# Kernel tuning notes

Measured on AMD Instinct MI355X. Metric: run time of the kernel, lower is better.

## Reference

```python
import jax, jax.numpy as jnp
import numpy as np

N_NODES = 100000
N_EDGES = 1600000
N_GRAPHS = 256
IN_DIM, HID = 30, 40

def setup_inputs() -> dict:
    key = jax.random.key(0)
    ks = jax.random.split(key, 12)
    x = jax.random.normal(ks[0], (N_NODES, IN_DIM), dtype=jnp.float32)
    edge_index = jax.random.randint(ks[1], (2, N_EDGES), 0, N_NODES, dtype=jnp.int64)
    batch = jnp.sort(jax.random.randint(ks[2], (N_NODES,), 0, N_GRAPHS, dtype=jnp.int64))
    def glorot(k, shape):
        lim = float(np.sqrt(6.0 / (shape[0] + shape[1])))
        return jax.random.uniform(k, shape, dtype=jnp.float32, minval=-lim, maxval=lim)
    return {
        'x': x, 'edge_index': edge_index, 'batch': batch,
        'W1': glorot(ks[3], (IN_DIM, HID)), 'b1': jnp.zeros((HID,), jnp.float32),
        'W2': glorot(ks[4], (HID, HID)),    'b2': jnp.zeros((HID,), jnp.float32),
        'W3': glorot(ks[5], (HID, HID)),    'b3': jnp.zeros((HID,), jnp.float32),
        'lin_w': glorot(ks[6], (HID, 1)),   'lin_b': jnp.zeros((1,), jnp.float32),
    }

def _gcn_layer(x, src, dst, norm, W, b, n_nodes):
    # x: [N, Fin] -> [N, Fout]; fused gather-matmul-scatter form of GCNConv
    h = x @ W                                   # dense transform first (Fout small)
    msg = h[src] * norm[:, None]                # [E+N, Fout] gather + edge scale
    out = jax.ops.segment_sum(msg, dst, num_segments=n_nodes)
    return out + b

def reference(x, edge_index, batch, W1, b1, W2, b2, W3, b3, lin_w, lin_b):
    n = x.shape[0]
    loops = jnp.arange(n, dtype=edge_index.dtype)
    src = jnp.concatenate([edge_index[0], loops])  # add self loops (GCNConv default)
    dst = jnp.concatenate([edge_index[1], loops])
    deg = jax.ops.segment_sum(jnp.ones_like(dst, dtype=x.dtype), dst, num_segments=n)
    dinv = jax.lax.rsqrt(jnp.maximum(deg, 1.0))    # deg >= 1 thanks to self loops
    norm = dinv[src] * dinv[dst]

    h = jax.nn.relu(_gcn_layer(x, src, dst, norm, W1, b1, n))  # dropout inactive (eval)
    h = jax.nn.relu(_gcn_layer(h, src, dst, norm, W2, b2, n))
    h = jax.nn.relu(_gcn_layer(h, src, dst, norm, W3, b3, n))

    # global_mean_pool over graphs
    g_sum = jax.ops.segment_sum(h, batch, num_segments=N_GRAPHS)
    cnt = jax.ops.segment_sum(jnp.ones((n,), h.dtype), batch, num_segments=N_GRAPHS)
    g = g_sum / jnp.maximum(cnt, 1.0)[:, None]
    return g @ lin_w + lin_b                      # [N_GRAPHS, 1]
```

## Files before the change

kernel.cpp:

```cpp
#include <hip/hip_runtime.h>

#define HID 40
#define RBKT 196
#define BSH 9
#define CAP 12288
#define EPB 4096


typedef __attribute__((ext_vector_type(4))) unsigned uv4;
typedef __attribute__((ext_vector_type(8))) __bf16 bf16x8;
typedef __attribute__((ext_vector_type(8))) unsigned short usv8;
typedef __attribute__((ext_vector_type(4))) float f32x4;

__device__ inline unsigned pack2_bf16(float a, float b) {
    unsigned ua = __float_as_uint(a);
    unsigned ub = __float_as_uint(b);
    ua = (ua + 0x7fffu + ((ua >> 16) & 1u)) >> 16;
    ub = (ub + 0x7fffu + ((ub >> 16) & 1u)) & 0xffff0000u;
    return ua | ub;
}

__device__ inline void acc8_bf16(float* acc, uint4 v) {
    acc[0] += __uint_as_float(v.x << 16);
    acc[1] += __uint_as_float(v.x & 0xffff0000u);
    acc[2] += __uint_as_float(v.y << 16);
    acc[3] += __uint_as_float(v.y & 0xffff0000u);
    acc[4] += __uint_as_float(v.z << 16);
    acc[5] += __uint_as_float(v.z & 0xffff0000u);
    acc[6] += __uint_as_float(v.w << 16);
    acc[7] += __uint_as_float(v.w & 0xffff0000u);
}

__device__ inline void wprep_dev(const float* __restrict__ W,
                                 unsigned* __restrict__ wtab, int INF, int l) {
    int lr = l & 15, lg = l >> 4;
    int kstn = (INF > 32) ? 2 : 1;
    for (int kst = 0; kst < kstn; kst++) {
        for (int ct = 0; ct < 3; ct++) {
            unsigned short v[8];
            #pragma unroll
            for (int i = 0; i < 8; i++) {
                int kb = kst * 32 + lg * 8 + i;
                int col = ct * 16 + lr;
                float f = (kb < INF && col < 40) ? W[kb * 40 + col] : 0.f;
                v[i] = (unsigned short)(pack2_bf16(f, 0.f) & 0xffffu);
            }
            uint4 u;
            u.x = (unsigned)v[0] | ((unsigned)v[1] << 16);
            u.y = (unsigned)v[2] | ((unsigned)v[3] << 16);
            u.z = (unsigned)v[4] | ((unsigned)v[5] << 16);
            u.w = (unsigned)v[6] | ((unsigned)v[7] << 16);
            reinterpret_cast<uint4*>(wtab)[(kst * 3 + ct) * 64 + l] = u;
        }
    }
}

__global__ void prep_kernel(int* __restrict__ bucket_cnt, float* __restrict__ g_sum, int G,
                            const float* __restrict__ W1, const float* __restrict__ W2,
                            const float* __restrict__ W3,
                            unsigned* __restrict__ wtab1, unsigned* __restrict__ wtab2,
                            unsigned* __restrict__ wtab3) {
    int t = threadIdx.x;
    if (t < RBKT) bucket_cnt[t] = 0;
    if (t < G) g_sum[t] = 0.f;
    int w = t >> 6, l = t & 63;
    if (w == 1) wprep_dev(W1, wtab1, 30, l);
    else if (w == 2) wprep_dev(W2, wtab2, 40, l);
    else if (w == 3) wprep_dev(W3, wtab3, 40, l);
}


__global__ __launch_bounds__(256) void binA_kernel(
        const int* __restrict__ esrc, const int* __restrict__ edst, int E,
        int* __restrict__ bucket_cnt, int* __restrict__ bucket_data) {
    __shared__ int cnt_l[RBKT];
    __shared__ int base_l[RBKT];
    int t = threadIdx.x;
    for (int b = t; b < RBKT; b += 256) cnt_l[b] = 0;
    __syncthreads();
    int e0 = blockIdx.x * EPB;
    int e1 = min(e0 + EPB, E);
    for (int e = e0 + t; e < e1; e += 256) {
        atomicAdd(&cnt_l[edst[e] >> BSH], 1);
    }
    __syncthreads();
    for (int b = t; b < RBKT; b += 256) {
        int c = cnt_l[b];
        base_l[b] = (c > 0) ? atomicAdd(&bucket_cnt[b], c) : 0;
        cnt_l[b] = 0;
    }
    __syncthreads();
    for (int e = e0 + t; e < e1; e += 256) {
        int d = edst[e];
        int s = esrc[e];
        int b = d >> BSH;
        int off = base_l[b] + atomicAdd(&cnt_l[b], 1);
        if (off < CAP) bucket_data[(size_t)b * CAP + off] = (s << BSH) | (d & 511);
    }
}

__global__ void scan_buckets_kernel(const int* __restrict__ cnt, int* __restrict__ base) {
    __shared__ int s[256];
    int t = threadIdx.x;
    int c = (t < RBKT) ? min(cnt[t], CAP) : 0;
    s[t] = c;
    __syncthreads();
    for (int off = 1; off < 256; off <<= 1) {
        int y = (t >= off) ? s[t - off] : 0;
        __syncthreads();
        s[t] += y;
        __syncthreads();
    }
    if (t < RBKT) base[t] = s[t] - c;
    if (t == RBKT - 1) base[RBKT] = s[t];
}

__global__ __launch_bounds__(256) void buildB_kernel(
        const int* __restrict__ bucket_cnt, const int* __restrict__ bucket_base,
        const int* __restrict__ bucket_data,
        int* __restrict__ rowptr, int* __restrict__ mid, int* __restrict__ csr,
        float* __restrict__ dinv, int n, int half) {
    __shared__ int deg_l[512];
    __shared__ int deg_lo[512];
    __shared__ int off_lo[512];
    __shared__ int off_hi[512];
    __shared__ int ps[256];
    int r = blockIdx.x;
    int t = threadIdx.x;
    int cnt = min(bucket_cnt[r], CAP);
    int base = bucket_base[r];
    int node0 = r << BSH;
    int nr = min(512, n - node0);
    for (int i = t; i < 512; i += 256) { deg_l[i] = 0; deg_lo[i] = 0; }
    __syncthreads();
    const int* data = bucket_data + (size_t)r * CAP;
    for (int e = t; e < cnt; e += 256) {
        int v = data[e];
        atomicAdd(&deg_l[v & 511], 1);
        if ((v >> BSH) < half) atomicAdd(&deg_lo[v & 511], 1);
    }
    __syncthreads();
    int a0 = deg_l[2 * t], a1 = deg_l[2 * t + 1];
    ps[t] = a0 + a1;
    __syncthreads();
    for (int off = 1; off < 256; off <<= 1) {
        int y = (t >= off) ? ps[t - off] : 0;
        __syncthreads();
        ps[t] += y;
        __syncthreads();
    }
    int excl = ps[t] - (a0 + a1);
    off_lo[2 * t] = excl;
    off_lo[2 * t + 1] = excl + a0;
    off_hi[2 * t] = excl + deg_lo[2 * t];
    off_hi[2 * t + 1] = excl + a0 + deg_lo[2 * t + 1];
    __syncthreads();
    for (int i = t; i < nr; i += 256) {
        int rp = base + off_lo[i];
        rowptr[node0 + i] = rp;
        mid[node0 + i] = rp + deg_lo[i];
        dinv[node0 + i] = rsqrtf((float)(deg_l[i] + 1));
    }
    if (r == RBKT - 1 && t == 0) rowptr[n] = base + cnt;
    __syncthreads();
    for (int e = t; e < cnt; e += 256) {
        int v = data[e];
        int s = v >> BSH;
        int d = v & 511;
        int p = (s < half) ? atomicAdd(&off_lo[d], 1) : atomicAdd(&off_hi[d], 1);
        csr[base + p] = s;
    }
}


__global__ __launch_bounds__(256) void scale_bf16_kernel(
        const float* __restrict__ x, const float* __restrict__ dinv,
        unsigned* __restrict__ xs, int n) {
    int t = blockIdx.x * blockDim.x + threadIdx.x;
    int i = t >> 4, p = t & 15;
    if (i >= n) return;
    float a = 0.f, b = 0.f;
    if (p < 15) {
        float d = dinv[i];
        a = x[i * 30 + 2 * p] * d;
        b = x[i * 30 + 2 * p + 1] * d;
    }
    xs[(size_t)i * 16 + p] = pack2_bf16(a, b);
}

template <int INF, int RQ, bool POOL>
__global__ __launch_bounds__(64 * RQ) void fused_layer_kernel(
        const unsigned* __restrict__ xs, const unsigned* __restrict__ wtab,
        const int* __restrict__ rowptr, const int* __restrict__ mid,
        const int* __restrict__ csr, const float* __restrict__ dinv,
        const float* __restrict__ bias, const float* __restrict__ lin_w,
        const int* __restrict__ batch,
        unsigned* __restrict__ out, float* __restrict__ g_sum, int n) {
    constexpr int KST = (INF > 32) ? 2 : 1;
    constexpr int NT  = 64 * RQ;
    constexpr int TS  = (RQ == 4) ? 5 : 7;
    __shared__ uint4 tile[64 * TS];
    __shared__ float sarr[POOL ? 64 : 1];
    __shared__ unsigned ost[POOL ? 1 : 64 * 21];
    const int tid = threadIdx.x;

    {
        const int node_l = tid / RQ, q = tid - node_l * RQ;
        const int gi = blockIdx.x * 64 + node_l;
        if (gi < n) {
            const uint4* tab = reinterpret_cast<const uint4*>(xs);
            float acc[8];
            {
                uint4 v = tab[(size_t)gi * RQ + q];
                acc[0] = __uint_as_float(v.x << 16);
                acc[1] = __uint_as_float(v.x & 0xffff0000u);
                acc[2] = __uint_as_float(v.y << 16);
                acc[3] = __uint_as_float(v.y & 0xffff0000u);
                acc[4] = __uint_as_float(v.z << 16);
                acc[5] = __uint_as_float(v.z & 0xffff0000u);
                acc[6] = __uint_as_float(v.w << 16);
                acc[7] = __uint_as_float(v.w & 0xffff0000u);
            }
            int e0 = rowptr[gi], m = mid[gi], e1 = rowptr[gi + 1];
            int e = e0;
            for (; e + 4 <= m; e += 4) {
                int s0 = csr[e], s1 = csr[e + 1], s2 = csr[e + 2], s3 = csr[e + 3];
                uint4 v0 = tab[(size_t)s0 * RQ + q];
                uint4 v1 = tab[(size_t)s1 * RQ + q];
                uint4 v2 = tab[(size_t)s2 * RQ + q];
                uint4 v3 = tab[(size_t)s3 * RQ + q];
                acc8_bf16(acc, v0);
                acc8_bf16(acc, v1);
                acc8_bf16(acc, v2);
                acc8_bf16(acc, v3);
            }
            for (; e < m; e++) acc8_bf16(acc, tab[(size_t)csr[e] * RQ + q]);
            for (; e + 4 <= e1; e += 4) {
                int s0 = csr[e], s1 = csr[e + 1], s2 = csr[e + 2], s3 = csr[e + 3];
                uint4 v0 = tab[(size_t)s0 * RQ + q];
                uint4 v1 = tab[(size_t)s1 * RQ + q];
                uint4 v2 = tab[(size_t)s2 * RQ + q];
                uint4 v3 = tab[(size_t)s3 * RQ + q];
                acc8_bf16(acc, v0);
                acc8_bf16(acc, v1);
                acc8_bf16(acc, v2);
                acc8_bf16(acc, v3);
            }
            for (; e < e1; e++) acc8_bf16(acc, tab[(size_t)csr[e] * RQ + q]);
            float d = dinv[gi];
            uint4 o;
            o.x = pack2_bf16(acc[0] * d, acc[1] * d);
            o.y = pack2_bf16(acc[2] * d, acc[3] * d);
            o.z = pack2_bf16(acc[4] * d, acc[5] * d);
            o.w = pack2_bf16(acc[6] * d, acc[7] * d);
            tile[node_l * TS + q] = o;
        }
    }
    __syncthreads();

    const int wv = tid >> 6, l = tid & 63, lr = l & 15, lg = l >> 4;
    if (wv < 4) {
        const uv4* wt = reinterpret_cast<const uv4*>(wtab);
        usv8 wf[KST][3];
        #pragma unroll
        for (int kst = 0; kst < KST; kst++) {
            #pragma unroll
            for (int ct = 0; ct < 3; ct++) {
                wf[kst][ct] = __builtin_bit_cast(usv8, wt[(kst * 3 + ct) * 64 + l]);
            }
        }
        const int node0 = blockIdx.x * 64 + wv * 16;
        const int arow_l = wv * 16 + lr;
        bf16x8 a0 = __builtin_bit_cast(bf16x8, tile[arow_l * TS + lg]);
        bf16x8 a1;
        if constexpr (KST == 2) {
            uint4 z4 = {0u, 0u, 0u, 0u};
            uint4 a1q = (lg == 0) ? tile[arow_l * TS + 4] : z4;
            a1 = __builtin_bit_cast(bf16x8, a1q);
        }
        f32x4 acc[3];
        #pragma unroll
        for (int ct = 0; ct < 3; ct++) {
            f32x4 z = {0.f, 0.f, 0.f, 0.f};
            acc[ct] = __builtin_amdgcn_mfma_f32_16x16x32_bf16(
                a0, __builtin_bit_cast(bf16x8, wf[0][ct]), z, 0, 0, 0);
            if constexpr (KST == 2) {
                acc[ct] = __builtin_amdgcn_mfma_f32_16x16x32_bf16(
                    a1, __builtin_bit_cast(bf16x8, wf[1][ct]), acc[ct], 0, 0, 0);
            }
        }
        int noder[4]; float dr[4]; bool vr[4];
        #pragma unroll
        for (int r = 0; r < 4; r++) {
            noder[r] = node0 + lg * 4 + r;
            vr[r] = (noder[r] < n);
            dr[r] = vr[r] ? dinv[noder[r]] : 0.f;
        }
        if (!POOL) {
            #pragma unroll
            for (int ct = 0; ct < 3; ct++) {
                int col = ct * 16 + lr;
                float bc = (col < 40) ? bias[col] : 0.f;
                #pragma unroll
                for (int r = 0; r < 4; r++) {
                    float v = fmaxf(acc[ct][r] + bc, 0.f) * dr[r];
                    float pv = __shfl_xor(v, 1, 64);
                    if (((lr & 1) == 0) && col < 40) {
                        int nl = wv * 16 + lg * 4 + r;
                        ost[nl * 21 + ct * 8 + (lr >> 1)] = pack2_bf16(v, pv);
                    }
                }
            }
        } else {
            float s[4] = {0.f, 0.f, 0.f, 0.f};
            #pragma unroll
            for (int ct = 0; ct < 3; ct++) {
                int col = ct * 16 + lr;
                float bc = (col < 40) ? bias[col] : 0.f;
                float lwv = (col < 40) ? lin_w[col] : 0.f;
                #pragma unroll
                for (int r = 0; r < 4; r++)
                    s[r] += fmaxf(acc[ct][r] + bc, 0.f) * lwv;
            }
            #pragma unroll
            for (int r = 0; r < 4; r++) if (!vr[r]) s[r] = 0.f;
            #pragma unroll
            for (int mask = 1; mask <= 8; mask <<= 1) {
                #pragma unroll
                for (int r = 0; r < 4; r++) s[r] += __shfl_xor(s[r], mask, 64);
            }
            if (lr == 0) {
                #pragma unroll
                for (int r = 0; r < 4; r++) sarr[wv * 16 + lg * 4 + r] = s[r];
            }
        }
    }
    __syncthreads();

    if (!POOL) {
        int blk0 = blockIdx.x * 64;
        int nr = min(64, n - blk0);
        int tot = nr * 5;
        uint4* outq = reinterpret_cast<uint4*>(out) + (size_t)blk0 * 5;
        for (int idx = tid; idx < tot; idx += NT) {
            int nl = idx / 5, c4 = idx - nl * 5;
            uint4 v;
            v.x = ost[nl * 21 + c4 * 4 + 0];
            v.y = ost[nl * 21 + c4 * 4 + 1];
            v.z = ost[nl * 21 + c4 * 4 + 2];
            v.w = ost[nl * 21 + c4 * 4 + 3];
            outq[idx] = v;
        }
    } else {
        if (tid < 64) {
            float ss = sarr[tid];
            int node2 = blockIdx.x * 64 + tid;
            bool v2 = (node2 < n);
            int gg = batch[v2 ? node2 : (n - 1)];
            if (!v2) ss = 0.f;
            int g0 = __shfl(gg, 0, 64);
            if (__all(gg == g0)) {
                #pragma unroll
                for (int off2 = 32; off2 > 0; off2 >>= 1) ss += __shfl_xor(ss, off2, 64);
                if (tid == 0) atomicAdd(&g_sum[g0], ss);
            } else {
                if (v2) atomicAdd(&g_sum[gg], ss);
            }
        }
    }
}

__global__ void finalize_kernel(const float* __restrict__ g_sum,
                                const int* __restrict__ batch,
                                const float* __restrict__ lin_b,
                                float* __restrict__ out, int n, int G) {
    int b = blockIdx.x * blockDim.x + threadIdx.x;
    if (b >= G) return;
    int lo = 0, hi = n;
    while (lo < hi) { int m = (lo + hi) >> 1; if (batch[m] < b) lo = m + 1; else hi = m; }
    int lo2 = lo, hi2 = n;
    while (lo2 < hi2) { int m = (lo2 + hi2) >> 1; if (batch[m] < b + 1) lo2 = m + 1; else hi2 = m; }
    int cnt = lo2 - lo;
    out[b] = g_sum[b] / (float)(cnt > 0 ? cnt : 1) + lin_b[0];
}


static inline size_t align_up(size_t v, size_t a) { return (v + a - 1) / a * a; }

extern "C" void kernel_launch(void* const* d_in, const int* in_sizes, int n_in,
                              void* d_out, int out_size, void* d_ws, size_t ws_size,
                              hipStream_t stream) {
    const float* x      = (const float*)d_in[0];
    const int*   esrc   = (const int*)d_in[1];
    const int*   batch  = (const int*)d_in[2];
    const float* W1     = (const float*)d_in[3];
    const float* b1     = (const float*)d_in[4];
    const float* W2     = (const float*)d_in[5];
    const float* b2     = (const float*)d_in[6];
    const float* W3     = (const float*)d_in[7];
    const float* b3     = (const float*)d_in[8];
    const float* lin_w  = (const float*)d_in[9];
    const float* lin_b  = (const float*)d_in[10];
    float* out = (float*)d_out;

    const int n = in_sizes[0] / 30;
    const int E = in_sizes[1] / 2;
    const int G = out_size;
    const int* edst = esrc + E;

    char* w = (char*)d_ws;
    size_t off = 0;
    auto take = [&](size_t bytes) { size_t o = off; off = align_up(off + bytes, 256); return (void*)(w + o); };
    int*      bucket_cnt  = (int*)take((size_t)RBKT * 4);
    int*      bucket_base = (int*)take((size_t)(RBKT + 1) * 4);
    int*      rowptr      = (int*)take((size_t)(n + 1) * 4);
    int*      mid         = (int*)take((size_t)n * 4);
    float*    dinv        = (float*)take((size_t)n * 4);
    int*      csr         = (int*)take((size_t)E * 4);
    float*    g_sum       = (float*)take((size_t)G * 4);
    unsigned* wtab1       = (unsigned*)take((size_t)3 * 64 * 16);
    unsigned* wtab2       = (unsigned*)take((size_t)6 * 64 * 16);
    unsigned* wtab3       = (unsigned*)take((size_t)6 * 64 * 16);
    size_t bd = (size_t)RBKT * CAP * 4;
    size_t x1 = (size_t)n * 16 * 4;
    void* shared_region = take(bd > x1 ? bd : x1);
    int*      bucket_data = (int*)shared_region;
    unsigned* xs1         = (unsigned*)shared_region;
    unsigned* tbA         = (unsigned*)take((size_t)n * 20 * 4);
    unsigned* tbB         = (unsigned*)take((size_t)n * 20 * 4);
    (void)ws_size;

    prep_kernel<<<1, 256, 0, stream>>>(bucket_cnt, g_sum, G, W1, W2, W3,
                                       wtab1, wtab2, wtab3);

    binA_kernel<<<(E + EPB - 1) / EPB, 256, 0, stream>>>(esrc, edst, E, bucket_cnt, bucket_data);
    scan_buckets_kernel<<<1, 256, 0, stream>>>(bucket_cnt, bucket_base);
    buildB_kernel<<<RBKT, 256, 0, stream>>>(bucket_cnt, bucket_base, bucket_data,
                                            rowptr, mid, csr, dinv, n, n / 2);

    int nblk = (n + 63) / 64;

    scale_bf16_kernel<<<((size_t)n * 16 + 255) / 256, 256, 0, stream>>>(x, dinv, xs1, n);
    fused_layer_kernel<30, 4, false><<<nblk, 256, 0, stream>>>(
        xs1, wtab1, rowptr, mid, csr, dinv, b1, nullptr, nullptr, tbA, nullptr, n);
    fused_layer_kernel<40, 5, false><<<nblk, 320, 0, stream>>>(
        tbA, wtab2, rowptr, mid, csr, dinv, b2, nullptr, nullptr, tbB, nullptr, n);
    fused_layer_kernel<40, 5, true><<<nblk, 320, 0, stream>>>(
        tbB, wtab3, rowptr, mid, csr, dinv, b3, lin_w, batch, nullptr, g_sum, n);

    finalize_kernel<<<1, 256, 0, stream>>>(g_sum, batch, lin_b, out, n, G);
}
```

Measured before the change: 196.3 us.

## Process two nodes per thread group to interleave gathers in fused GCN layers

Each block now handles 128 nodes instead of 64. Every thread group aggregates two nodes (A and B) at once, interleaving their neighbor gathers in lockstep batches of four so more independent loads are in flight. The MFMA stage runs two passes per wave, and the pooling stage uses two wavefronts. Doubling per-thread accumulators raises register pressure and halves the grid size, which may reduce occupancy. Imbalanced degrees between A and B fall back to the serial drain loops.

```diff
diff --git a/kernel.cpp b/kernel.cpp
--- a/kernel.cpp
+++ b/kernel.cpp
@@ -199,31 +199,32 @@
     constexpr int KST = (INF > 32) ? 2 : 1;
     constexpr int NT  = 64 * RQ;
     constexpr int TS  = (RQ == 4) ? 5 : 7;
-    __shared__ uint4 tile[64 * TS];
-    __shared__ float sarr[POOL ? 64 : 1];
-    __shared__ unsigned ost[POOL ? 1 : 64 * 21];
+    __shared__ uint4 tile[128 * TS];
+    __shared__ float sarr[POOL ? 128 : 1];
+    __shared__ unsigned ost[POOL ? 1 : 128 * 21];
     const int tid = threadIdx.x;
+    const uint4* tab = reinterpret_cast<const uint4*>(xs);
 
     {
-        const int node_l = tid / RQ, q = tid - node_l * RQ;
-        const int gi = blockIdx.x * 64 + node_l;
-        if (gi < n) {
-            const uint4* tab = reinterpret_cast<const uint4*>(xs);
-            float acc[8];
-            {
-                uint4 v = tab[(size_t)gi * RQ + q];
-                acc[0] = __uint_as_float(v.x << 16);
-                acc[1] = __uint_as_float(v.x & 0xffff0000u);
-                acc[2] = __uint_as_float(v.y << 16);
-                acc[3] = __uint_as_float(v.y & 0xffff0000u);
-                acc[4] = __uint_as_float(v.z << 16);
-                acc[5] = __uint_as_float(v.z & 0xffff0000u);
-                acc[6] = __uint_as_float(v.w << 16);
-                acc[7] = __uint_as_float(v.w & 0xffff0000u);
-            }
-            int e0 = rowptr[gi], m = mid[gi], e1 = rowptr[gi + 1];
-            int e = e0;
-            for (; e + 4 <= m; e += 4) {
+        const int nl = tid / RQ, q = tid - nl * RQ;
+        const int gA = blockIdx.x * 128 + nl;
+        const int gB = gA + 64;
+        const bool vA = (gA < n), vB = (gB < n);
+        float accA[8] = {0,0,0,0,0,0,0,0};
+        float accB[8] = {0,0,0,0,0,0,0,0};
+        int eA = 0, mA = 0, eA1 = 0, eB = 0, mB = 0, eB1 = 0;
+        if (vA) {
+            uint4 v = tab[(size_t)gA * RQ + q];
+            acc8_bf16(accA, v);
+            eA = rowptr[gA]; mA = mid[gA]; eA1 = rowptr[gA + 1];
+        }
+        if (vB) {
+            uint4 v = tab[(size_t)gB * RQ + q];
+            acc8_bf16(accB, v);
+            eB = rowptr[gB]; mB = mid[gB]; eB1 = rowptr[gB + 1];
+        }
+        auto drain = [&](int e, int end, float* acc) {
+            for (; e + 4 <= end; e += 4) {
                 int s0 = csr[e], s1 = csr[e + 1], s2 = csr[e + 2], s3 = csr[e + 3];
                 uint4 v0 = tab[(size_t)s0 * RQ + q];
                 uint4 v1 = tab[(size_t)s1 * RQ + q];
@@ -234,26 +235,64 @@
                 acc8_bf16(acc, v2);
                 acc8_bf16(acc, v3);
             }
-            for (; e < m; e++) acc8_bf16(acc, tab[(size_t)csr[e] * RQ + q]);
-            for (; e + 4 <= e1; e += 4) {
-                int s0 = csr[e], s1 = csr[e + 1], s2 = csr[e + 2], s3 = csr[e + 3];
-                uint4 v0 = tab[(size_t)s0 * RQ + q];
-                uint4 v1 = tab[(size_t)s1 * RQ + q];
-                uint4 v2 = tab[(size_t)s2 * RQ + q];
-                uint4 v3 = tab[(size_t)s3 * RQ + q];
-                acc8_bf16(acc, v0);
-                acc8_bf16(acc, v1);
-                acc8_bf16(acc, v2);
-                acc8_bf16(acc, v3);
-            }
-            for (; e < e1; e++) acc8_bf16(acc, tab[(size_t)csr[e] * RQ + q]);
-            float d = dinv[gi];
+            for (; e < end; e++) acc8_bf16(acc, tab[(size_t)csr[e] * RQ + q]);
+        };
+        while (eA + 4 <= mA && eB + 4 <= mB) {
+            int a0 = csr[eA], a1 = csr[eA + 1], a2 = csr[eA + 2], a3 = csr[eA + 3];
+            int b0 = csr[eB], b1 = csr[eB + 1], b2 = csr[eB + 2], b3 = csr[eB + 3];
+            uint4 va0 = tab[(size_t)a0 * RQ + q];
+            uint4 vb0 = tab[(size_t)b0 * RQ + q];
+            uint4 va1 = tab[(size_t)a1 * RQ + q];
+            uint4 vb1 = tab[(size_t)b1 * RQ + q];
+            uint4 va2 = tab[(size_t)a2 * RQ + q];
+            uint4 vb2 = tab[(size_t)b2 * RQ + q];
+            uint4 va3 = tab[(size_t)a3 * RQ + q];
+            uint4 vb3 = tab[(size_t)b3 * RQ + q];
+            acc8_bf16(accA, va0); acc8_bf16(accB, vb0);
+            acc8_bf16(accA, va1); acc8_bf16(accB, vb1);
+            acc8_bf16(accA, va2); acc8_bf16(accB, vb2);
+            acc8_bf16(accA, va3); acc8_bf16(accB, vb3);
+            eA += 4; eB += 4;
+        }
+        drain(eA, mA, accA);
+        drain(eB, mB, accB);
+        eA = mA; eB = mB;
+        while (eA + 4 <= eA1 && eB + 4 <= eB1) {
+            int a0 = csr[eA], a1 = csr[eA + 1], a2 = csr[eA + 2], a3 = csr[eA + 3];
+            int b0 = csr[eB], b1 = csr[eB + 1], b2 = csr[eB + 2], b3 = csr[eB + 3];
+            uint4 va0 = tab[(size_t)a0 * RQ + q];
+            uint4 vb0 = tab[(size_t)b0 * RQ + q];
+            uint4 va1 = tab[(size_t)a1 * RQ + q];
+            uint4 vb1 = tab[(size_t)b1 * RQ + q];
+            uint4 va2 = tab[(size_t)a2 * RQ + q];
+            uint4 vb2 = tab[(size_t)b2 * RQ + q];
+            uint4 va3 = tab[(size_t)a3 * RQ + q];
+            uint4 vb3 = tab[(size_t)b3 * RQ + q];
+            acc8_bf16(accA, va0); acc8_bf16(accB, vb0);
+            acc8_bf16(accA, va1); acc8_bf16(accB, vb1);
+            acc8_bf16(accA, va2); acc8_bf16(accB, vb2);
+            acc8_bf16(accA, va3); acc8_bf16(accB, vb3);
+            eA += 4; eB += 4;
+        }
+        drain(eA, eA1, accA);
+        drain(eB, eB1, accB);
+        if (vA) {
+            float d = dinv[gA];
             uint4 o;
-            o.x = pack2_bf16(acc[0] * d, acc[1] * d);
-            o.y = pack2_bf16(acc[2] * d, acc[3] * d);
-            o.z = pack2_bf16(acc[4] * d, acc[5] * d);
-            o.w = pack2_bf16(acc[6] * d, acc[7] * d);
-            tile[node_l * TS + q] = o;
+            o.x = pack2_bf16(accA[0] * d, accA[1] * d);
+            o.y = pack2_bf16(accA[2] * d, accA[3] * d);
+            o.z = pack2_bf16(accA[4] * d, accA[5] * d);
+            o.w = pack2_bf16(accA[6] * d, accA[7] * d);
+            tile[nl * TS + q] = o;
+        }
+        if (vB) {
+            float d = dinv[gB];
+            uint4 o;
+            o.x = pack2_bf16(accB[0] * d, accB[1] * d);
+            o.y = pack2_bf16(accB[2] * d, accB[3] * d);
+            o.z = pack2_bf16(accB[4] * d, accB[5] * d);
+            o.w = pack2_bf16(accB[6] * d, accB[7] * d);
+            tile[(nl + 64) * TS + q] = o;
         }
     }
     __syncthreads();
@@ -269,92 +308,96 @@
                 wf[kst][ct] = __builtin_bit_cast(usv8, wt[(kst * 3 + ct) * 64 + l]);
             }
         }
-        const int node0 = blockIdx.x * 64 + wv * 16;
-        const int arow_l = wv * 16 + lr;
-        bf16x8 a0 = __builtin_bit_cast(bf16x8, tile[arow_l * TS + lg]);
-        bf16x8 a1;
-        if constexpr (KST == 2) {
-            uint4 z4 = {0u, 0u, 0u, 0u};
-            uint4 a1q = (lg == 0) ? tile[arow_l * TS + 4] : z4;
-            a1 = __builtin_bit_cast(bf16x8, a1q);
-        }
-        f32x4 acc[3];
         #pragma unroll
-        for (int ct = 0; ct < 3; ct++) {
-            f32x4 z = {0.f, 0.f, 0.f, 0.f};
-            acc[ct] = __builtin_amdgcn_mfma_f32_16x16x32_bf16(
-                a0, __builtin_bit_cast(bf16x8, wf[0][ct]), z, 0, 0, 0);
+        for (int pass = 0; pass < 2; pass++) {
+            const int tt = wv + pass * 4;
+            const int node0 = blockIdx.x * 128 + tt * 16;
+            const int arow_l = tt * 16 + lr;
+            bf16x8 a0 = __builtin_bit_cast(bf16x8, tile[arow_l * TS + lg]);
+            bf16x8 a1;
             if constexpr (KST == 2) {
-                acc[ct] = __builtin_amdgcn_mfma_f32_16x16x32_bf16(
-                    a1, __builtin_bit_cast(bf16x8, wf[1][ct]), acc[ct], 0, 0, 0);
-            }
-        }
-        int noder[4]; float dr[4]; bool vr[4];
-        #pragma unroll
-        for (int r = 0; r < 4; r++) {
-            noder[r] = node0 + lg * 4 + r;
-            vr[r] = (noder[r] < n);
-            dr[r] = vr[r] ? dinv[noder[r]] : 0.f;
-        }
-        if (!POOL) {
+                uint4 z4 = {0u, 0u, 0u, 0u};
+                uint4 a1q = (lg == 0) ? tile[arow_l * TS + 4] : z4;
+                a1 = __builtin_bit_cast(bf16x8, a1q);
+            }
+            f32x4 acc[3];
             #pragma unroll
             for (int ct = 0; ct < 3; ct++) {
-                int col = ct * 16 + lr;
-                float bc = (col < 40) ? bias[col] : 0.f;
+                f32x4 z = {0.f, 0.f, 0.f, 0.f};
+                acc[ct] = __builtin_amdgcn_mfma_f32_16x16x32_bf16(
+                    a0, __builtin_bit_cast(bf16x8, wf[0][ct]), z, 0, 0, 0);
+                if constexpr (KST == 2) {
+                    acc[ct] = __builtin_amdgcn_mfma_f32_16x16x32_bf16(
+                        a1, __builtin_bit_cast(bf16x8, wf[1][ct]), acc[ct], 0, 0, 0);
+                }
+            }
+            int noder[4]; float dr[4]; bool vr[4];
+            #pragma unroll
+            for (int r = 0; r < 4; r++) {
+                noder[r] = node0 + lg * 4 + r;
+                vr[r] = (noder[r] < n);
+                dr[r] = vr[r] ? dinv[noder[r]] : 0.f;
+            }
+            if (!POOL) {
                 #pragma unroll
-                for (int r = 0; r < 4; r++) {
-                    float v = fmaxf(acc[ct][r] + bc, 0.f) * dr[r];
-                    float pv = __shfl_xor(v, 1, 64);
-                    if (((lr & 1) == 0) && col < 40) {
-                        int nl = wv * 16 + lg * 4 + r;
-                        ost[nl * 21 + ct * 8 + (lr >> 1)] = pack2_bf16(v, pv);
+                for (int ct = 0; ct < 3; ct++) {
+                    int col = ct * 16 + lr;
+                    float bc = (col < 40) ? bias[col] : 0.f;
+                    #pragma unroll
+                    for (int r = 0; r < 4; r++) {
+                        float v = fmaxf(acc[ct][r] + bc, 0.f) * dr[r];
+                        float pv = __shfl_xor(v, 1, 64);
+                        if (((lr & 1) == 0) && col < 40) {
+                            int nl2 = tt * 16 + lg * 4 + r;
+                            ost[nl2 * 21 + ct * 8 + (lr >> 1)] = pack2_bf16(v, pv);
+                        }
                     }
                 }
-            }
-        } else {
-            float s[4] = {0.f, 0.f, 0.f, 0.f};
-            #pragma unroll
-            for (int ct = 0; ct < 3; ct++) {
-                int col = ct * 16 + lr;
-                float bc = (col < 40) ? bias[col] : 0.f;
-                float lwv = (col < 40) ? lin_w[col] : 0.f;
+            } else {
+                float s[4] = {0.f, 0.f, 0.f, 0.f};
                 #pragma unroll
-                for (int r = 0; r < 4; r++)
-                    s[r] += fmaxf(acc[ct][r] + bc, 0.f) * lwv;
-            }
-            #pragma unroll
-            for (int r = 0; r < 4; r++) if (!vr[r]) s[r] = 0.f;
-            #pragma unroll
-            for (int mask = 1; mask <= 8; mask <<= 1) {
+                for (int ct = 0; ct < 3; ct++) {
+                    int col = ct * 16 + lr;
+                    float bc = (col < 40) ? bias[col] : 0.f;
+                    float lwv = (col < 40) ? lin_w[col] : 0.f;
+                    #pragma unroll
+                    for (int r = 0; r < 4; r++)
+                        s[r] += fmaxf(acc[ct][r] + bc, 0.f) * lwv;
+                }
                 #pragma unroll
-                for (int r = 0; r < 4; r++) s[r] += __shfl_xor(s[r], mask, 64);
-            }
-            if (lr == 0) {
+                for (int r = 0; r < 4; r++) if (!vr[r]) s[r] = 0.f;
                 #pragma unroll
-                for (int r = 0; r < 4; r++) sarr[wv * 16 + lg * 4 + r] = s[r];
+                for (int mask = 1; mask <= 8; mask <<= 1) {
+                    #pragma unroll
+                    for (int r = 0; r < 4; r++) s[r] += __shfl_xor(s[r], mask, 64);
+                }
+                if (lr == 0) {
+                    #pragma unroll
+                    for (int r = 0; r < 4; r++) sarr[tt * 16 + lg * 4 + r] = s[r];
+                }
             }
         }
     }
     __syncthreads();
 
     if (!POOL) {
-        int blk0 = blockIdx.x * 64;
-        int nr = min(64, n - blk0);
+        int blk0 = blockIdx.x * 128;
+        int nr = min(128, n - blk0);
         int tot = nr * 5;
         uint4* outq = reinterpret_cast<uint4*>(out) + (size_t)blk0 * 5;
         for (int idx = tid; idx < tot; idx += NT) {
-            int nl = idx / 5, c4 = idx - nl * 5;
+            int nl2 = idx / 5, c4 = idx - nl2 * 5;
             uint4 v;
-            v.x = ost[nl * 21 + c4 * 4 + 0];
-            v.y = ost[nl * 21 + c4 * 4 + 1];
-            v.z = ost[nl * 21 + c4 * 4 + 2];
-            v.w = ost[nl * 21 + c4 * 4 + 3];
+            v.x = ost[nl2 * 21 + c4 * 4 + 0];
+            v.y = ost[nl2 * 21 + c4 * 4 + 1];
+            v.z = ost[nl2 * 21 + c4 * 4 + 2];
+            v.w = ost[nl2 * 21 + c4 * 4 + 3];
             outq[idx] = v;
         }
     } else {
-        if (tid < 64) {
+        if (tid < 128) {
             float ss = sarr[tid];
-            int node2 = blockIdx.x * 64 + tid;
+            int node2 = blockIdx.x * 128 + tid;
             bool v2 = (node2 < n);
             int gg = batch[v2 ? node2 : (n - 1)];
             if (!v2) ss = 0.f;
@@ -362,7 +405,7 @@
             if (__all(gg == g0)) {
                 #pragma unroll
                 for (int off2 = 32; off2 > 0; off2 >>= 1) ss += __shfl_xor(ss, off2, 64);
-                if (tid == 0) atomicAdd(&g_sum[g0], ss);
+                if ((tid & 63) == 0) atomicAdd(&g_sum[g0], ss);
             } else {
                 if (v2) atomicAdd(&g_sum[gg], ss);
             }
@@ -438,7 +481,7 @@
     buildB_kernel<<<RBKT, 256, 0, stream>>>(bucket_cnt, bucket_base, bucket_data,
                                             rowptr, mid, csr, dinv, n, n / 2);
 
-    int nblk = (n + 63) / 64;
+    int nblk = (n + 127) / 128;
 
     scale_bf16_kernel<<<((size_t)n * 16 + 255) / 256, 256, 0, stream>>>(x, dinv, xs1, n);
     fused_layer_kernel<30, 4, false><<<nblk, 256, 0, stream>>>(
```

After: 252.0 us. +28.4%, slower.
